# Kernel tuning notes

Hardware: AMD Instinct MI355X
Metric: run time of the kernel (lower is better)

## Reference

```python
import jax, jax.numpy as jnp
import numpy as np

EPSILON = 1e-6
MINMAX_RATIO = 20 ** 0.5
N_NODES, N_EDGES = 60000, 240000
WIDTH, NUM_HEAD, DIM_HEAD = 256, 8, 32
WIDTH_NORM = NUM_HEAD * DIM_HEAD          # 256
WIDTH_ACT = NUM_HEAD * DIM_HEAD * 4       # 1024
EDGE_VOCAB, EDGE_FEATS = 16, 3


def _inv_softplus(y):
    return np.log(np.expm1(y))


def setup_inputs() -> dict:
    key = jax.random.key(0)
    ks = jax.random.split(key, 16)
    inp = {
        'x': jax.random.normal(ks[0], (N_NODES, WIDTH), jnp.float32),
        'deg': jax.random.randint(ks[1], (N_NODES,), 0, 6, jnp.int32),
        'edge_idx': jax.random.randint(ks[2], (2, N_EDGES), 0, N_NODES, jnp.int32),
        'edge_attr': jax.random.randint(ks[3], (N_EDGES, EDGE_FEATS), 0, EDGE_VOCAB, jnp.int32),
        'node_elec': jax.random.normal(ks[4], (N_NODES, 2), jnp.float32),
        # parameters (init scales per module code)
        'lora_down': jax.random.normal(ks[5], (WIDTH, DIM_HEAD)) / np.sqrt(WIDTH),
        # original init is zeros; small random values used so this path is exercised
        'lora_up': jax.random.normal(ks[6], (DIM_HEAD, WIDTH_NORM)) * 0.01,
        'emb_edge': jax.random.normal(ks[7], (EDGE_VOCAB, DIM_HEAD)) * (0.01 / np.sqrt(EDGE_FEATS)),
        'moa_w': jnp.zeros((2, DIM_HEAD), jnp.float32),
        'moa_s': jnp.tile(jnp.linspace(float(_inv_softplus(0.1)), float(_inv_softplus(10.0)), DIM_HEAD), (2, 1)),
        'elec_lin': jax.random.normal(ks[8], (2, DIM_HEAD)) * (0.01 / np.sqrt(2)),
        'emb_deg': jax.random.normal(ks[9], (6, WIDTH_NORM)) * 0.1,
        'lin_pre': jax.random.normal(ks[10], (WIDTH, WIDTH_NORM)) / np.sqrt(WIDTH),
        'gate_lin': jax.random.normal(ks[11], (WIDTH_NORM, WIDTH_NORM)) / np.sqrt(WIDTH_NORM),
        'gate_kernel': jax.random.normal(ks[12], (NUM_HEAD, DIM_HEAD, DIM_HEAD * 4)) / np.sqrt(DIM_HEAD),
        'value_lin': jax.random.normal(ks[13], (WIDTH_NORM, WIDTH_NORM)) / np.sqrt(WIDTH_NORM),
        'value_kernel': jax.random.normal(ks[14], (NUM_HEAD, DIM_HEAD, DIM_HEAD * 4)) / np.sqrt(DIM_HEAD),
        'act_bias': jnp.full((WIDTH_ACT,), float(_inv_softplus(0.5)), jnp.float32),
        'post_kernel': jax.random.normal(ks[15], (NUM_HEAD, DIM_HEAD * 4, DIM_HEAD)) / np.sqrt(DIM_HEAD * 4),
    }
    return inp


def _clip_with_grad(x, lo, hi):
    return jax.lax.stop_gradient(jnp.clip(x, lo, hi) - x) + x


def _group_linear(x, lin_kernel, head_kernel, norm_bias=None):
    H, D, F = head_kernel.shape
    xx = (x @ lin_kernel).reshape(*x.shape[:-1], H, D)
    xx = xx / jnp.sqrt(jnp.mean(jnp.square(xx), axis=-1, keepdims=True) + EPSILON)
    if norm_bias is not None:
        xx = (xx + norm_bias.reshape(xx.shape)) / 2 ** 0.5
    xx = jnp.einsum('nhd,hdf->nhf', xx, head_kernel)
    return xx.reshape(*x.shape[:-1], H * F)


def reference(x, deg, edge_idx, edge_attr, node_elec, lora_down, lora_up, emb_edge,
              moa_w, moa_s, elec_lin, emb_deg, lin_pre, gate_lin, gate_kernel,
              value_lin, value_kernel, act_bias, post_kernel):
    ei0, ei1 = edge_idx[0], edge_idx[1]
    # edge embedding: bond features + electronegativity difference (MoAct tanh mixture)
    diff = node_elec[ei0] - node_elec[ei1]                      # [E,2]
    w = jax.nn.softplus(moa_w)
    w = w / w.sum(axis=-1, keepdims=True)
    s = jax.nn.softplus(moa_s)
    moa_out = (jnp.tanh(diff[..., None] * s) * w).sum(-1)       # [E,2]
    emb = jnp.sum(emb_edge[edge_attr], axis=-2) + moa_out @ elec_lin  # [E,dim_head]
    # per-edge message with LoRA modulation, scatter-add to destination nodes
    msg = x[ei0] + x[ei1]                                       # [E,width]
    msg = msg @ lin_pre + ((msg @ lora_down) * emb) @ lora_up   # [E,width_norm]
    agg = jax.ops.segment_sum(msg, ei1, num_segments=x.shape[0])
    # gated post-block with degree-embedding gate bias
    gate_bias = emb_deg[deg]                                    # [N,width_norm]
    gg = _group_linear(agg, gate_lin, gate_kernel, gate_bias)   # [N,width_act]
    vv = _group_linear(agg, value_lin, value_kernel)
    a = jax.nn.softplus(gg + act_bias)
    a = _clip_with_grad(a, 1.0 / MINMAX_RATIO, MINMAX_RATIO)
    xx = (a * vv).reshape(agg.shape[0], NUM_HEAD, -1)           # [N,H,4*dim_head]
    xx = jnp.einsum('nhd,hdf->nhf', xx, post_kernel)
    return xx.reshape(agg.shape[0], -1)                         # [N,width_norm]
```

## Files before the change

### kernel.cpp

```cpp
#include <hip/hip_runtime.h>
#include <hip/hip_bf16.h>

typedef unsigned short u16;

#define NN 60000
#define NE 240000

typedef __attribute__((ext_vector_type(8))) short bfrag;
typedef __attribute__((ext_vector_type(4))) float ffrag;

__device__ __forceinline__ float bf2f(u16 u) {
    union { unsigned int i; float f; } v; v.i = ((unsigned int)u) << 16; return v.f;
}
__device__ __forceinline__ u16 f2bf(float f) {
    __hip_bfloat16 h = __float2bfloat16(f);
    return *reinterpret_cast<u16*>(&h);
}
__device__ __forceinline__ float softplusf(float x) {
    return fmaxf(x, 0.f) + log1pf(expf(-fabsf(x)));
}
__device__ __forceinline__ float fast_softplus(float x) {
    return __logf(1.f + __expf(x));
}
__device__ __forceinline__ float fast_sp_clip(float x) {
    float a = __logf(1.f + __expf(x));
    return fminf(fmaxf(a, 0.22360679774997896f), 4.47213595499957939f);
}
__device__ __forceinline__ float fast_tanh(float x) {
    float t = __expf(fminf(fmaxf(2.f * x, -30.f), 30.f));
    return (t - 1.f) * __builtin_amdgcn_rcpf(t + 1.f);
}
template<bool B>
__device__ __forceinline__ float LD(const void* p, int i) {
    if constexpr (B) return bf2f(((const u16*)p)[i]);
    else             return ((const float*)p)[i];
}
__device__ __forceinline__ bfrag ldfrag(const u16* p) {
    return *reinterpret_cast<const bfrag*>(p);
}
__device__ __forceinline__ ffrag MFMA(bfrag a, bfrag b, ffrag c) {
    return __builtin_amdgcn_mfma_f32_16x16x32_bf16(a, b, c, 0, 0, 0);
}

__global__ void detect_kernel(const u16* __restrict__ x, int* __restrict__ flag) {
    __shared__ int cnt;
    if (threadIdx.x == 0) cnt = 0;
    __syncthreads();
    int c = 0;
    for (int i = threadIdx.x; i < 2048; i += 256) {
        u16 w = x[2 * i];
        int e = (w >> 7) & 0xFF;
        if (e >= 112 && e <= 143) c++;
    }
    atomicAdd(&cnt, c);
    __syncthreads();
    if (threadIdx.x == 0) *flag = (cnt > 1024) ? 1 : 0;
}

template<bool B>
__device__ void prep_body(const void* gate_lin, const void* value_lin,
    const void* lin_pre, const void* lora_down, const void* lora_up,
    const void* gate_kernel, const void* value_kernel, const void* post_kernel,
    u16* gT, u16* vT, u16* lpT, u16* ldT, u16* luT, u16* gkT, u16* vkT, u16* pkT,
    int tid, int stride)
{
    for (int i = tid; i < 65536; i += stride) {
        int n = i >> 8, k = i & 255;
        gT[i]  = f2bf(LD<B>(gate_lin,  k * 256 + n));
        vT[i]  = f2bf(LD<B>(value_lin, k * 256 + n));
        lpT[i] = f2bf(LD<B>(lin_pre,   k * 256 + n));
    }
    for (int i = tid; i < 8192; i += stride) {
        { int n = i >> 8, k = i & 255; ldT[i] = f2bf(LD<B>(lora_down, k * 32 + n)); }
        { int n = i >> 5, k = i & 31;  luT[i] = f2bf(LD<B>(lora_up,   k * 256 + n)); }
    }
    for (int i = tid; i < 32768; i += stride) {
        { int hf = i >> 5, d = i & 31, h = hf >> 7, f = hf & 127;
          gkT[i] = f2bf(LD<B>(gate_kernel,  h * 4096 + d * 128 + f));
          vkT[i] = f2bf(LD<B>(value_kernel, h * 4096 + d * 128 + f)); }
        { int hd = i >> 7, f = i & 127, h = hd >> 5, d2 = hd & 31;
          pkT[i] = f2bf(LD<B>(post_kernel, h * 4096 + f * 32 + d2)); }
    }
}
__global__ void prep_kernel(const void* gate_lin, const void* value_lin,
    const void* lin_pre, const void* lora_down, const void* lora_up,
    const void* gate_kernel, const void* value_kernel, const void* post_kernel,
    u16* gT, u16* vT, u16* lpT, u16* ldT, u16* luT, u16* gkT, u16* vkT, u16* pkT,
    const int* flag)
{
    int tid = blockIdx.x * blockDim.x + threadIdx.x;
    int stride = gridDim.x * blockDim.x;
    if (*flag) prep_body<true >(gate_lin, value_lin, lin_pre, lora_down, lora_up,
        gate_kernel, value_kernel, post_kernel, gT, vT, lpT, ldT, luT, gkT, vkT, pkT, tid, stride);
    else       prep_body<false>(gate_lin, value_lin, lin_pre, lora_down, lora_up,
        gate_kernel, value_kernel, post_kernel, gT, vT, lpT, ldT, luT, gkT, vkT, pkT, tid, stride);
}


struct PreSmem { __align__(16) u16 xB[64][264]; };

template<bool B>
__device__ void pre_body(PreSmem& sm, const void* x, const u16* ldT,
                         u16* xb, u16* xd, int blk, int j)
{
    const int w = j >> 6, quad = (j >> 4) & 3, l15 = j & 15;
    {
        int row = j >> 2, seg = j & 3, c0 = seg * 64;
        int gr = blk * 64 + row;
        if (gr < NN) {
            if constexpr (B) {
                const u16* xp = (const u16*)x + (size_t)gr * 256 + c0;
                for (int cc = 0; cc < 64; cc += 8)
                    *reinterpret_cast<bfrag*>(&sm.xB[row][c0 + cc]) = ldfrag(xp + cc);
            } else {
                const float* xp = (const float*)x + (size_t)gr * 256 + c0;
                u16* xbp = xb + (size_t)gr * 256 + c0;
                for (int cc = 0; cc < 64; cc += 8) {
                    float4 v0 = *(const float4*)(xp + cc);
                    float4 v1 = *(const float4*)(xp + cc + 4);
                    bfrag o;
                    o[0] = (short)f2bf(v0.x); o[1] = (short)f2bf(v0.y);
                    o[2] = (short)f2bf(v0.z); o[3] = (short)f2bf(v0.w);
                    o[4] = (short)f2bf(v1.x); o[5] = (short)f2bf(v1.y);
                    o[6] = (short)f2bf(v1.z); o[7] = (short)f2bf(v1.w);
                    *reinterpret_cast<bfrag*>(&sm.xB[row][c0 + cc]) = o;
                    *reinterpret_cast<bfrag*>(xbp + cc) = o;
                }
            }
        } else {
            bfrag z = {0,0,0,0,0,0,0,0};
            for (int cc = 0; cc < 64; cc += 8)
                *reinterpret_cast<bfrag*>(&sm.xB[row][c0 + cc]) = z;
        }
    }
    __syncthreads();
    const int r0 = w * 16;
    bfrag A[8];
    #pragma unroll
    for (int kt = 0; kt < 8; kt++)
        A[kt] = ldfrag(&sm.xB[r0 + l15][kt * 32 + quad * 8]);

    #pragma unroll
    for (int t = 0; t < 2; t++) {
        int n0 = t * 16;
        ffrag acc = {0.f, 0.f, 0.f, 0.f};
        #pragma unroll
        for (int kt = 0; kt < 8; kt++)
            acc = MFMA(A[kt], ldfrag(ldT + (n0 + l15) * 256 + kt * 32 + quad * 8), acc);
        #pragma unroll
        for (int r = 0; r < 4; r++) {
            int gr = blk * 64 + r0 + quad * 4 + r;
            if (gr < NN) xd[(size_t)gr * 32 + n0 + l15] = f2bf(acc[r]);
        }
    }
}
__global__ __launch_bounds__(256) void pre_kernel(const void* x, const u16* ldT,
    u16* xb, u16* xd, const int* flag)
{
    __shared__ PreSmem sm;
    const int j = threadIdx.x, blk = blockIdx.x;
    if (*flag) pre_body<true >(sm, x, ldT, xb, xd, blk, j);
    else       pre_body<false>(sm, x, ldT, xb, xd, blk, j);
}

__global__ __launch_bounds__(256) void hist_kernel(const int* __restrict__ edge_idx,
                                                   int* __restrict__ cnt)
{
    int e = blockIdx.x * blockDim.x + threadIdx.x;
    int stride = gridDim.x * blockDim.x;
    for (; e < NE; e += stride) atomicAdd(&cnt[edge_idx[NE + e]], 1);
}

__global__ __launch_bounds__(256) void scanA_kernel(const int* __restrict__ cnt,
                                                    int* __restrict__ bsum)
{
    __shared__ int sd[256];
    int b = blockIdx.x, j = threadIdx.x;
    int base = b * 1024 + j * 4;
    int s = 0;
    #pragma unroll
    for (int k = 0; k < 4; k++) { int i = base + k; if (i < NN) s += cnt[i]; }
    sd[j] = s; __syncthreads();
    for (int st = 128; st > 0; st >>= 1) {
        if (j < st) sd[j] += sd[j + st];
        __syncthreads();
    }
    if (j == 0) bsum[b] = sd[0];
}

__global__ __launch_bounds__(256) void scanB_kernel(const int* __restrict__ cnt,
    const int* __restrict__ bsum, int* __restrict__ off, int* __restrict__ cur)
{
    __shared__ int sd[256];
    int b = blockIdx.x, j = threadIdx.x;
    int pre = 0;
    for (int k = 0; k < b; k++) pre += bsum[k];
    int base = b * 1024 + j * 4;
    int c[4]; int tsum = 0;
    #pragma unroll
    for (int k = 0; k < 4; k++) { int i = base + k; c[k] = (i < NN) ? cnt[i] : 0; tsum += c[k]; }
    sd[j] = tsum; __syncthreads();
    for (int st = 1; st < 256; st <<= 1) {
        int v = (j >= st) ? sd[j - st] : 0;
        __syncthreads();
        sd[j] += v;
        __syncthreads();
    }
    int excl = sd[j] - tsum;
    int run = pre + excl;
    #pragma unroll
    for (int k = 0; k < 4; k++) {
        int i = base + k;
        if (i < NN) { off[i] = run; cur[i] = run; }
        run += c[k];
    }
}

struct EdgeWSmem {
    float wL[64], sL[64];
    float embT[512];
    float elT[64];
};

template<bool B>
__device__ void edgew_body(EdgeWSmem& sm, const int* edge_idx, const int* edge_attr,
    const void* node_elec, const void* emb_edge, const void* moa_w, const void* moa_s,
    const void* elec_lin, const u16* xd, u16* W, int* srcL, int* cur, int g, int j)
{
    if (j < 64) {
        int c = j >> 5;
        float sw = fast_softplus(LD<B>(moa_w, j));
        float tot = 0.f;
        #pragma unroll
        for (int d = 0; d < 32; d++) tot += fast_softplus(LD<B>(moa_w, c * 32 + d));
        sm.wL[j] = sw / tot;
        sm.sL[j] = fast_softplus(LD<B>(moa_s, j));
        sm.elT[j] = LD<B>(elec_lin, j);
    }
    for (int i = j; i < 512; i += 256) sm.embT[i] = LD<B>(emb_edge, i);
    __syncthreads();

    const int t = j & 3, s = j >> 2, e = g * 64 + s;
    const int a = edge_idx[e], b = edge_idx[NE + e];
    const int ch = t >> 1, dr = (t & 1) * 16;
    float df = LD<B>(node_elec, a * 2 + ch) - LD<B>(node_elec, b * 2 + ch);
    float part = 0.f;
    #pragma unroll
    for (int d = 0; d < 16; d++) {
        int dd = ch * 32 + dr + d;
        part += fast_tanh(df * sm.sL[dd]) * sm.wL[dd];
    }
    part += __shfl_xor(part, 1);
    int base = (j & 63) & ~3;
    float moa0 = __shfl(part, base + 0);
    float moa1 = __shfl(part, base + 2);

    int a0 = edge_attr[e * 3 + 0], a1 = edge_attr[e * 3 + 1], a2 = edge_attr[e * 3 + 2];
    int d0 = t * 8;
    bfrag va = ldfrag(xd + (size_t)a * 32 + d0);
    bfrag vb = ldfrag(xd + (size_t)b * 32 + d0);
    bfrag o;
    #pragma unroll
    for (int q = 0; q < 8; q++) {
        int d = d0 + q;
        float emb = sm.embT[a0 * 32 + d] + sm.embT[a1 * 32 + d] + sm.embT[a2 * 32 + d]
                  + moa0 * sm.elT[d] + moa1 * sm.elT[32 + d];
        o[q] = (short)f2bf((bf2f((u16)va[q]) + bf2f((u16)vb[q])) * emb);
    }
    int slot = 0;
    if (t == 0) slot = atomicAdd(&cur[b], 1);
    slot = __shfl(slot, base);
    if (t == 0) srcL[slot] = a;
    *reinterpret_cast<bfrag*>(W + (size_t)slot * 32 + d0) = o;
}

__global__ __launch_bounds__(256) void edgew_kernel(const int* edge_idx,
    const int* edge_attr, const void* node_elec, const void* emb_edge,
    const void* moa_w, const void* moa_s, const void* elec_lin,
    const u16* xd, u16* W, int* srcL, int* cur, const int* flag)
{
    __shared__ EdgeWSmem sm;
    const int j = threadIdx.x, g = blockIdx.x;
    if (*flag) edgew_body<true >(sm, edge_idx, edge_attr, node_elec, emb_edge,
                                 moa_w, moa_s, elec_lin, xd, W, srcL, cur, g, j);
    else       edgew_body<false>(sm, edge_idx, edge_attr, node_elec, emb_edge,
                                 moa_w, moa_s, elec_lin, xd, W, srcL, cur, g, j);
}

struct NodeSmemF {
    __align__(16) union U1 {
        u16 aggB[16][264];
        u16 ghatB[16][264];
    } u1;
    __align__(16) u16 sB[16][264];
    __align__(16) u16 xxW[4][16][136];
    __align__(16) u16 uB[16][40];
    int srcC[192];
    int degL[16], offL[16], idgL[16];
};

template<bool B>
__device__ void node_body_f(NodeSmemF& sm, const void* x, const u16* xb,
    const u16* Wb, const int* srcL, const int* off, const int* cnt, const int* deg,
    const void* emb_deg, const void* act_bias, const u16* gT, const u16* vT,
    const u16* gkT, const u16* vkT, const u16* pkT, const u16* lpT, const u16* luT,
    void* out, int blk, int j)
{
    const int w = j >> 6, quad = (j >> 4) & 3, l15 = j & 15;
    const int n0g = blk * 16;
    const u16* xbp = B ? (const u16*)x : xb;

    int o0 = off[n0g];
    int eb = off[n0g + 15] + cnt[n0g + 15] - o0;
    if (j < 192 && j < eb) sm.srcC[j] = srcL[o0 + j];
    if (j < 16) {
        sm.degL[j] = deg[n0g + j];
        sm.offL[j] = off[n0g + j];
        sm.idgL[j] = cnt[n0g + j];
    }
    __syncthreads();

    {
        int s = j >> 4, dp = j & 15, c0 = dp * 16;
        int o = sm.offL[s], dg = sm.idgL[s], base = o - o0;
        float acc[16];
        #pragma unroll
        for (int k = 0; k < 16; k++) acc[k] = 0.f;
        float u0 = 0.f, u1 = 0.f;
        bfrag pv0 = {0,0,0,0,0,0,0,0}, pv1 = {0,0,0,0,0,0,0,0};
        float pw0 = 0.f, pw1 = 0.f;
        if (dg > 0) {
            int src = (base < 192) ? sm.srcC[base] : srcL[o];
            const u16* xr = xbp + (size_t)src * 256 + c0;
            pv0 = ldfrag(xr); pv1 = ldfrag(xr + 8);
            const u16* wr = Wb + (size_t)o * 32 + dp;
            pw0 = bf2f(wr[0]); pw1 = bf2f(wr[16]);
        }
        for (int i = 0; i < dg; i++) {
            bfrag v0 = pv0, v1 = pv1;
            float w0 = pw0, w1 = pw1;
            if (i + 1 < dg) {
                int idx = base + i + 1;
                int src = (idx < 192) ? sm.srcC[idx] : srcL[o + i + 1];
                const u16* xr = xbp + (size_t)src * 256 + c0;
                pv0 = ldfrag(xr); pv1 = ldfrag(xr + 8);
                const u16* wr = Wb + (size_t)(o + i + 1) * 32 + dp;
                pw0 = bf2f(wr[0]); pw1 = bf2f(wr[16]);
            }
            u0 += w0; u1 += w1;
            #pragma unroll
            for (int q = 0; q < 8; q++) {
                acc[q]     += bf2f((u16)v0[q]);
                acc[q + 8] += bf2f((u16)v1[q]);
            }
        }
        {
            const u16* xr = xbp + (size_t)(n0g + s) * 256 + c0;
            bfrag v0 = ldfrag(xr), v1 = ldfrag(xr + 8);
            float fd = (float)dg;
            #pragma unroll
            for (int q = 0; q < 8; q++) {
                acc[q]     = fmaf(fd, bf2f((u16)v0[q]), acc[q]);
                acc[q + 8] = fmaf(fd, bf2f((u16)v1[q]), acc[q + 8]);
            }
        }
        sm.uB[s][dp] = f2bf(u0); sm.uB[s][dp + 16] = f2bf(u1);
        #pragma unroll
        for (int cq = 0; cq < 16; cq += 2) {
            unsigned int pv = (unsigned int)f2bf(acc[cq]) | ((unsigned int)f2bf(acc[cq + 1]) << 16);
            *reinterpret_cast<unsigned int*>(&sm.sB[s][c0 + cq]) = pv;
        }
    }
    __syncthreads();

    {
        bfrag S[8];
        #pragma unroll
        for (int kt = 0; kt < 8; kt++)
            S[kt] = ldfrag(&sm.sB[l15][kt * 32 + quad * 8]);
        bfrag uA = ldfrag(&sm.uB[l15][quad * 8]);
        #pragma unroll
        for (int tt = 0; tt < 4; tt++) {
            int n0 = (w * 4 + tt) * 16;
            const u16* bp = lpT + (n0 + l15) * 256 + quad * 8;
            bfrag b0 = ldfrag(bp +   0), b1 = ldfrag(bp +  32),
                  b2 = ldfrag(bp +  64), b3 = ldfrag(bp +  96),
                  b4 = ldfrag(bp + 128), b5 = ldfrag(bp + 160),
                  b6 = ldfrag(bp + 192), b7 = ldfrag(bp + 224);
            bfrag lu = ldfrag(luT + (n0 + l15) * 32 + quad * 8);
            ffrag acc = {0.f, 0.f, 0.f, 0.f};
            acc = MFMA(S[0], b0, acc); acc = MFMA(S[1], b1, acc);
            acc = MFMA(S[2], b2, acc); acc = MFMA(S[3], b3, acc);
            acc = MFMA(S[4], b4, acc); acc = MFMA(S[5], b5, acc);
            acc = MFMA(S[6], b6, acc); acc = MFMA(S[7], b7, acc);
            acc = MFMA(uA, lu, acc);
            #pragma unroll
            for (int r = 0; r < 4; r++)
                sm.u1.aggB[quad * 4 + r][n0 + l15] = f2bf(acc[r]);
        }
    }
    __syncthreads();

    {
        bfrag A[8];
        #pragma unroll
        for (int kt = 0; kt < 8; kt++)
            A[kt] = ldfrag(&sm.u1.aggB[l15][kt * 32 + quad * 8]);
        __syncthreads();

        const bool isG = (w >> 1) == 0;
        const u16* WT = isG ? gT : vT;
        const int half = (w & 1) * 128;
        #pragma unroll
        for (int hd = 0; hd < 4; hd++) {
            int n0 = half + hd * 32;
            ffrag a0 = {0.f, 0.f, 0.f, 0.f}, a1 = {0.f, 0.f, 0.f, 0.f};
            {
                const u16* bp = WT + (n0 + l15) * 256 + quad * 8;
                bfrag b0 = ldfrag(bp +   0), b1 = ldfrag(bp +  32),
                      b2 = ldfrag(bp +  64), b3 = ldfrag(bp +  96),
                      b4 = ldfrag(bp + 128), b5 = ldfrag(bp + 160),
                      b6 = ldfrag(bp + 192), b7 = ldfrag(bp + 224);
                a0 = MFMA(A[0], b0, a0); a0 = MFMA(A[1], b1, a0);
                a0 = MFMA(A[2], b2, a0); a0 = MFMA(A[3], b3, a0);
                a0 = MFMA(A[4], b4, a0); a0 = MFMA(A[5], b5, a0);
                a0 = MFMA(A[6], b6, a0); a0 = MFMA(A[7], b7, a0);
            }
            {
                const u16* bp = WT + (n0 + 16 + l15) * 256 + quad * 8;
                bfrag b0 = ldfrag(bp +   0), b1 = ldfrag(bp +  32),
                      b2 = ldfrag(bp +  64), b3 = ldfrag(bp +  96),
                      b4 = ldfrag(bp + 128), b5 = ldfrag(bp + 160),
                      b6 = ldfrag(bp + 192), b7 = ldfrag(bp + 224);
                a1 = MFMA(A[0], b0, a1); a1 = MFMA(A[1], b1, a1);
                a1 = MFMA(A[2], b2, a1); a1 = MFMA(A[3], b3, a1);
                a1 = MFMA(A[4], b4, a1); a1 = MFMA(A[5], b5, a1);
                a1 = MFMA(A[6], b6, a1); a1 = MFMA(A[7], b7, a1);
            }
            float inv[4];
            #pragma unroll
            for (int r = 0; r < 4; r++) {
                float sq = a0[r] * a0[r] + a1[r] * a1[r];
                sq += __shfl_xor(sq, 1);
                sq += __shfl_xor(sq, 2);
                sq += __shfl_xor(sq, 4);
                sq += __shfl_xor(sq, 8);
                inv[r] = 1.f / sqrtf(sq * (1.f / 32.f) + 1e-6f);
            }
            if (isG) {
                #pragma unroll
                for (int r = 0; r < 4; r++) {
                    int row = quad * 4 + r;
                    int dgr = sm.degL[row];
                    float b0 = LD<B>(emb_deg, dgr * 256 + n0 + l15);
                    float b1 = LD<B>(emb_deg, dgr * 256 + n0 + 16 + l15);
                    sm.u1.ghatB[row][n0 + l15] =
                        f2bf((a0[r] * inv[r] + b0) * 0.70710678118654752f);
                    sm.u1.ghatB[row][n0 + 16 + l15] =
                        f2bf((a1[r] * inv[r] + b1) * 0.70710678118654752f);
                }
            } else {
                #pragma unroll
                for (int r = 0; r < 4; r++) {
                    int row = quad * 4 + r;
                    sm.sB[row][n0 + l15]      = f2bf(a0[r] * inv[r]);
                    sm.sB[row][n0 + 16 + l15] = f2bf(a1[r] * inv[r]);
                }
            }
        }
    }
    __syncthreads();

    u16 (*xxW)[136] = sm.xxW[w];
    #pragma unroll
    for (int hh = 0; hh < 2; hh++) {
        int h = w * 2 + hh;
        bfrag aG = ldfrag(&sm.u1.ghatB[l15][h * 32 + quad * 8]);
        bfrag aV = ldfrag(&sm.sB[l15][h * 32 + quad * 8]);
        #pragma unroll
        for (int t = 0; t < 8; t++) {
            int n0 = t * 16;
            bfrag bg = ldfrag(gkT + (h * 128 + n0 + l15) * 32 + quad * 8);
            bfrag bv = ldfrag(vkT + (h * 128 + n0 + l15) * 32 + quad * 8);
            ffrag zero = {0.f, 0.f, 0.f, 0.f};
            ffrag ag = MFMA(aG, bg, zero);
            ffrag av = MFMA(aV, bv, zero);
            float bias = LD<B>(act_bias, h * 128 + n0 + l15);
            #pragma unroll
            for (int r = 0; r < 4; r++) {
                float a = fast_sp_clip(ag[r] + bias);
                xxW[quad * 4 + r][n0 + l15] = f2bf(a * av[r]);
            }
        }
        bfrag A4[4];
        #pragma unroll
        for (int kt = 0; kt < 4; kt++)
            A4[kt] = ldfrag(&xxW[l15][kt * 32 + quad * 8]);
        #pragma unroll
        for (int t = 0; t < 2; t++) {
            int n0 = t * 16;
            const u16* pp = pkT + (h * 32 + n0 + l15) * 128 + quad * 8;
            bfrag c0 = ldfrag(pp), c1 = ldfrag(pp + 32),
                  c2 = ldfrag(pp + 64), c3 = ldfrag(pp + 96);
            ffrag acc = {0.f, 0.f, 0.f, 0.f};
            acc = MFMA(A4[0], c0, acc); acc = MFMA(A4[1], c1, acc);
            acc = MFMA(A4[2], c2, acc); acc = MFMA(A4[3], c3, acc);
            #pragma unroll
            for (int r = 0; r < 4; r++) {
                size_t idx = (size_t)(n0g + quad * 4 + r) * 256 + h * 32 + n0 + l15;
                if constexpr (B) ((u16*)out)[idx] = f2bf(acc[r]);
                else             ((float*)out)[idx] = acc[r];
            }
        }
    }
}

__global__ __launch_bounds__(256, 4) void node_kernel_f(
    const void* x, const u16* xb, const u16* Wb, const int* srcL, const int* off,
    const int* cnt, const int* deg, const void* emb_deg, const void* act_bias,
    const u16* gT, const u16* vT, const u16* gkT, const u16* vkT, const u16* pkT,
    const u16* lpT, const u16* luT, void* out, const int* flag)
{
    __shared__ NodeSmemF sm;
    const int j = threadIdx.x, blk = blockIdx.x;
    if (*flag) node_body_f<true >(sm, x, xb, Wb, srcL, off, cnt, deg, emb_deg, act_bias,
                                  gT, vT, gkT, vkT, pkT, lpT, luT, out, blk, j);
    else       node_body_f<false>(sm, x, xb, Wb, srcL, off, cnt, deg, emb_deg, act_bias,
                                  gT, vT, gkT, vkT, pkT, lpT, luT, out, blk, j);
}

struct EdgeSmemM {
    __align__(16) u16 msgB[64][264];
    __align__(16) u16 uB[64][40];
    __align__(16) float embL[64][32];
    float wL[64], sL[64];
    float moaL[64][2];
    int ei0s[64], ei1s[64];
};

template<bool B>
__device__ void edge_body_m(EdgeSmemM& sm, const void* x, const int* edge_idx,
    const int* edge_attr, const void* node_elec, const void* emb_edge,
    const void* moa_w, const void* moa_s, const void* elec_lin,
    const u16* ldT, const u16* luT, const u16* lpT, float* agg, int g, int j)
{
    const int w = j >> 6, quad = (j >> 4) & 3, l15 = j & 15;
    const int lane = j & 63;

    if (w == 0) {
        int c = lane >> 5;
        float sw = softplusf(LD<B>(moa_w, lane));
        float tot = 0.f;
        #pragma unroll
        for (int d = 0; d < 32; d++) tot += softplusf(LD<B>(moa_w, c * 32 + d));
        sm.wL[lane] = sw / tot;
        sm.sL[lane] = softplusf(LD<B>(moa_s, lane));
        int e = g * 64 + lane;
        int a = edge_idx[e], b = edge_idx[NE + e];
        sm.ei0s[lane] = a; sm.ei1s[lane] = b;
        #pragma unroll
        for (int c2 = 0; c2 < 2; c2++) {
            float df = LD<B>(node_elec, a * 2 + c2) - LD<B>(node_elec, b * 2 + c2);
            float acc = 0.f;
            for (int d = 0; d < 32; d++)
                acc += tanhf(df * sm.sL[c2 * 32 + d]) * sm.wL[c2 * 32 + d];
            sm.moaL[lane][c2] = acc;
        }
    }
    __syncthreads();

    {
        int row = j >> 2, seg = j & 3, c0 = seg * 64;
        int e0 = sm.ei0s[row], e1 = sm.ei1s[row];
        if constexpr (B) {
            const u16* xp = (const u16*)x;
            for (int cc = 0; cc < 64; cc += 8) {
                bfrag v0 = ldfrag(xp + (size_t)e0 * 256 + c0 + cc);
                bfrag v1 = ldfrag(xp + (size_t)e1 * 256 + c0 + cc);
                bfrag o;
                #pragma unroll
                for (int q = 0; q < 8; q++)
                    o[q] = (short)f2bf(bf2f((u16)v0[q]) + bf2f((u16)v1[q]));
                *reinterpret_cast<bfrag*>(&sm.msgB[row][c0 + cc]) = o;
            }
        } else {
            const float* xp = (const float*)x;
            for (int cc = 0; cc < 64; cc += 4) {
                float4 v0 = *(const float4*)(xp + (size_t)e0 * 256 + c0 + cc);
                float4 v1 = *(const float4*)(xp + (size_t)e1 * 256 + c0 + cc);
                ushort4 o = { f2bf(v0.x + v1.x), f2bf(v0.y + v1.y),
                              f2bf(v0.z + v1.z), f2bf(v0.w + v1.w) };
                *reinterpret_cast<ushort4*>(&sm.msgB[row][c0 + cc]) = o;
            }
        }
        int e = row, d0 = seg * 8, ea = g * 64 + e;
        int a0 = edge_attr[ea * 3 + 0], a1 = edge_attr[ea * 3 + 1], a2 = edge_attr[ea * 3 + 2];
        float m0 = sm.moaL[e][0], m1 = sm.moaL[e][1];
        #pragma unroll
        for (int d = d0; d < d0 + 8; d++) {
            sm.embL[e][d] = LD<B>(emb_edge, a0 * 32 + d) + LD<B>(emb_edge, a1 * 32 + d)
                          + LD<B>(emb_edge, a2 * 32 + d)
                          + m0 * LD<B>(elec_lin, d) + m1 * LD<B>(elec_lin, 32 + d);
        }
    }
    __syncthreads();

    const int r0 = w * 16;
    bfrag A[8];
    #pragma unroll
    for (int kt = 0; kt < 8; kt++)
        A[kt] = ldfrag(&sm.msgB[r0 + l15][kt * 32 + quad * 8]);

    #pragma unroll
    for (int t = 0; t < 2; t++) {
        int n0 = t * 16;
        ffrag acc = {0.f, 0.f, 0.f, 0.f};
        #pragma unroll
        for (int kt = 0; kt < 8; kt++)
            acc = MFMA(A[kt], ldfrag(ldT + (n0 + l15) * 256 + kt * 32 + quad * 8), acc);
        #pragma unroll
        for (int r = 0; r < 4; r++) {
            int row = r0 + quad * 4 + r;
            sm.uB[row][n0 + l15] = f2bf(acc[r] * sm.embL[row][n0 + l15]);
        }
    }
    bfrag uA = ldfrag(&sm.uB[r0 + l15][quad * 8]);

    int er[4];
    #pragma unroll
    for (int r = 0; r < 4; r++) er[r] = sm.ei1s[r0 + quad * 4 + r];

    for (int t = 0; t < 16; t++) {
        int n0 = t * 16;
        ffrag acc = {0.f, 0.f, 0.f, 0.f};
        #pragma unroll
        for (int kt = 0; kt < 8; kt++)
            acc = MFMA(A[kt], ldfrag(lpT + (n0 + l15) * 256 + kt * 32 + quad * 8), acc);
        acc = MFMA(uA, ldfrag(luT + (n0 + l15) * 32 + quad * 8), acc);
        #pragma unroll
        for (int r = 0; r < 4; r++)
            unsafeAtomicAdd(&agg[(size_t)er[r] * 256 + n0 + l15], acc[r]);
    }
}

__global__ __launch_bounds__(256) void edge_kernel_m(
    const void* x, const int* edge_idx, const int* edge_attr,
    const void* node_elec, const void* emb_edge, const void* moa_w,
    const void* moa_s, const void* elec_lin,
    const u16* ldT, const u16* luT, const u16* lpT, float* agg, const int* flag)
{
    __shared__ EdgeSmemM sm;
    const int j = threadIdx.x, g = blockIdx.x;
    if (*flag) edge_body_m<true >(sm, x, edge_idx, edge_attr, node_elec, emb_edge,
                                  moa_w, moa_s, elec_lin, ldT, luT, lpT, agg, g, j);
    else       edge_body_m<false>(sm, x, edge_idx, edge_attr, node_elec, emb_edge,
                                  moa_w, moa_s, elec_lin, ldT, luT, lpT, agg, g, j);
}

struct NodeSmemM {
    union U1 {
        u16 aggB[16][264];
        u16 ghatB[16][264];
    } u1;
    union U2 {
        struct P { float gF[16][260]; float vF[16][260]; } p;
        u16 xxB[16][1032];
    } u2;
    __align__(16) u16 vhatB[16][264];
    float grmsL[16][8], vrmsL[16][8];
    int degL[16];
};

template<bool B>
__device__ void node_body_m(NodeSmemM& sm, const float* agg, const int* deg,
    const void* emb_deg, const void* act_bias, const u16* gT, const u16* vT,
    const u16* gkT, const u16* vkT, const u16* pkT, void* out, int blk, int j)
{
    const int w = j >> 6, quad = (j >> 4) & 3, l15 = j & 15;
    const int n0g = blk * 16;

// ... 206 lines not shown
    for (int s = 0; s < 8; s++)
        unsafeAtomicAdd(&agg[(size_t)sm.ei1s[s] * 256 + j], acc[s]);
}

__global__ __launch_bounds__(256) void edge_kernel_fb(
    const void* x, const int* edge_idx, const int* edge_attr,
    const void* node_elec, const void* lora_down, const void* lora_up,
    const void* emb_edge, const void* moa_w, const void* moa_s,
    const void* elec_lin, const void* lin_pre, float* agg, const int* flag)
{
    __shared__ EdgeSmemFB sm;
    const int j = threadIdx.x, g = blockIdx.x;
    if (*flag) edge_body_fb<true >(sm, x, edge_idx, edge_attr, node_elec, lora_down,
                                   lora_up, emb_edge, moa_w, moa_s, elec_lin, lin_pre, agg, g, j);
    else       edge_body_fb<false>(sm, x, edge_idx, edge_attr, node_elec, lora_down,
                                   lora_up, emb_edge, moa_w, moa_s, elec_lin, lin_pre, agg, g, j);
}

struct NodeSmemFB {
    __align__(16) float aggT[256][8];
    float gL[8][256];
    float vL[8][256];
    float ghat[256], vhat[256];
    float xxL[1024];
};

template<bool B>
__device__ void node_body_fb(NodeSmemFB& sm,
    const float* agg, const int* deg, const void* emb_deg,
    const void* gate_lin, const void* value_lin, const void* gate_kernel,
    const void* value_kernel, const void* act_bias, const void* post_kernel,
    void* out, int n0, int j)
{
    #pragma unroll
    for (int s = 0; s < 8; s++) sm.aggT[j][s] = agg[(size_t)(n0 + s) * 256 + j];
    __syncthreads();

    float ga[8], va[8];
    #pragma unroll
    for (int s = 0; s < 8; s++) { ga[s] = 0.f; va[s] = 0.f; }
    #pragma unroll 4
    for (int k = 0; k < 256; k++) {
        float wg = LD<B>(gate_lin,  k * 256 + j);
        float wv = LD<B>(value_lin, k * 256 + j);
        const float4 a0 = *reinterpret_cast<const float4*>(&sm.aggT[k][0]);
        const float4 a1 = *reinterpret_cast<const float4*>(&sm.aggT[k][4]);
        ga[0] = fmaf(a0.x, wg, ga[0]); va[0] = fmaf(a0.x, wv, va[0]);
        ga[1] = fmaf(a0.y, wg, ga[1]); va[1] = fmaf(a0.y, wv, va[1]);
        ga[2] = fmaf(a0.z, wg, ga[2]); va[2] = fmaf(a0.z, wv, va[2]);
        ga[3] = fmaf(a0.w, wg, ga[3]); va[3] = fmaf(a0.w, wv, va[3]);
        ga[4] = fmaf(a1.x, wg, ga[4]); va[4] = fmaf(a1.x, wv, va[4]);
        ga[5] = fmaf(a1.y, wg, ga[5]); va[5] = fmaf(a1.y, wv, va[5]);
        ga[6] = fmaf(a1.z, wg, ga[6]); va[6] = fmaf(a1.z, wv, va[6]);
        ga[7] = fmaf(a1.w, wg, ga[7]); va[7] = fmaf(a1.w, wv, va[7]);
    }
    __syncthreads();
    #pragma unroll
    for (int s = 0; s < 8; s++) { sm.gL[s][j] = ga[s]; sm.vL[s][j] = va[s]; }

    const int h = j >> 5, dd = j & 31, f0 = dd << 2;
    const float lo = 0.22360679774997896f, hi = 4.47213595499957939f;

    for (int s = 0; s < 8; s++) {
        __syncthreads();
        float gs = 0.f, vs = 0.f;
        #pragma unroll
        for (int d = 0; d < 32; d++) {
            float g = sm.gL[s][h * 32 + d];
            float v = sm.vL[s][h * 32 + d];
            gs = fmaf(g, g, gs); vs = fmaf(v, v, vs);
        }
        float grms = sqrtf(gs * (1.f / 32.f) + 1e-6f);
        float vrms = sqrtf(vs * (1.f / 32.f) + 1e-6f);
        float gv = sm.gL[s][j], vv = sm.vL[s][j];
        float bias = LD<B>(emb_deg, deg[n0 + s] * 256 + j);
        sm.ghat[j] = (gv / grms + bias) * 0.70710678118654752f;
        sm.vhat[j] = vv / vrms;
        __syncthreads();

        float a0 = 0.f, a1 = 0.f, a2 = 0.f, a3 = 0.f;
        float b0 = 0.f, b1 = 0.f, b2 = 0.f, b3 = 0.f;
        #pragma unroll 4
        for (int d = 0; d < 32; d++) {
            float gh = sm.ghat[h * 32 + d];
            float vh = sm.vhat[h * 32 + d];
            int base = h * 4096 + d * 128 + f0;
            a0 = fmaf(gh, LD<B>(gate_kernel,  base + 0), a0);
            a1 = fmaf(gh, LD<B>(gate_kernel,  base + 1), a1);
            a2 = fmaf(gh, LD<B>(gate_kernel,  base + 2), a2);
            a3 = fmaf(gh, LD<B>(gate_kernel,  base + 3), a3);
            b0 = fmaf(vh, LD<B>(value_kernel, base + 0), b0);
            b1 = fmaf(vh, LD<B>(value_kernel, base + 1), b1);
            b2 = fmaf(vh, LD<B>(value_kernel, base + 2), b2);
            b3 = fmaf(vh, LD<B>(value_kernel, base + 3), b3);
        }
        int fb = h * 128 + f0;
        a0 = fminf(fmaxf(softplusf(a0 + LD<B>(act_bias, fb + 0)), lo), hi);
        a1 = fminf(fmaxf(softplusf(a1 + LD<B>(act_bias, fb + 1)), lo), hi);
        a2 = fminf(fmaxf(softplusf(a2 + LD<B>(act_bias, fb + 2)), lo), hi);
        a3 = fminf(fmaxf(softplusf(a3 + LD<B>(act_bias, fb + 3)), lo), hi);
        sm.xxL[fb + 0] = a0 * b0; sm.xxL[fb + 1] = a1 * b1;
        sm.xxL[fb + 2] = a2 * b2; sm.xxL[fb + 3] = a3 * b3;
        __syncthreads();

        float o = 0.f;
        #pragma unroll 4
        for (int f = 0; f < 128; f++)
            o = fmaf(sm.xxL[h * 128 + f], LD<B>(post_kernel, h * 4096 + f * 32 + dd), o);
        if constexpr (B) ((u16*)out)[(size_t)(n0 + s) * 256 + j] = f2bf(o);
        else             ((float*)out)[(size_t)(n0 + s) * 256 + j] = o;
    }
}

__global__ __launch_bounds__(256) void node_kernel_fb(
    const float* agg, const int* deg, const void* emb_deg,
    const void* gate_lin, const void* value_lin, const void* gate_kernel,
    const void* value_kernel, const void* act_bias, const void* post_kernel,
    void* out, const int* flag)
{
    __shared__ NodeSmemFB sm;
    const int j = threadIdx.x, n0 = blockIdx.x * 8;
    if (*flag) node_body_fb<true >(sm, agg, deg, emb_deg, gate_lin, value_lin,
                                   gate_kernel, value_kernel, act_bias, post_kernel, out, n0, j);
    else       node_body_fb<false>(sm, agg, deg, emb_deg, gate_lin, value_lin,
                                   gate_kernel, value_kernel, act_bias, post_kernel, out, n0, j);
}

extern "C" void kernel_launch(void* const* d_in, const int* in_sizes, int n_in,
                              void* d_out, int out_size, void* d_ws, size_t ws_size,
                              hipStream_t stream) {
    const void* x           = d_in[0];
    const int*  deg         = (const int*)d_in[1];
    const int*  edge_idx    = (const int*)d_in[2];
    const int*  edge_attr   = (const int*)d_in[3];
    const void* node_elec   = d_in[4];
    const void* lora_down   = d_in[5];
    const void* lora_up     = d_in[6];
    const void* emb_edge    = d_in[7];
    const void* moa_w       = d_in[8];
    const void* moa_s       = d_in[9];
    const void* elec_lin    = d_in[10];
    const void* emb_deg     = d_in[11];
    const void* lin_pre     = d_in[12];
    const void* gate_lin    = d_in[13];
    const void* gate_kernel = d_in[14];
    const void* value_lin   = d_in[15];
    const void* value_kernel= d_in[16];
    const void* act_bias    = d_in[17];
    const void* post_kernel = d_in[18];

    const size_t AGG_BYTES = (size_t)NN * 256 * 4;
    const size_t T_BYTES   = (size_t)(3 * 65536 + 2 * 8192 + 3 * 32768) * 2;

    const size_t XB_OFF  = 16 + T_BYTES;
    const size_t W_OFF   = XB_OFF  + (size_t)NN * 256 * 2;
    const size_t XD_OFF  = W_OFF   + (size_t)NE * 32 * 2;
    const size_t SRC_OFF = XD_OFF  + (size_t)NN * 32 * 2;
    const size_t CNT_OFF = SRC_OFF + (size_t)NE * 4;
    const size_t OFF_OFF = CNT_OFF + (size_t)NN * 4;
    const size_t CUR_OFF = OFF_OFF + (size_t)NN * 4;
    const size_t BS_OFF  = CUR_OFF + (size_t)NN * 4;
    const size_t NEW_NEEDED = BS_OFF + 256;

    const size_t T_OFF_OLD  = AGG_BYTES + 16;
    const size_t OLD_NEEDED = T_OFF_OLD + T_BYTES;

    if (ws_size >= NEW_NEEDED) {
        int* flag = (int*)d_ws;
        u16* gT  = (u16*)((char*)d_ws + 16);
        u16* vT  = gT  + 65536;
        u16* lpT = vT  + 65536;
        u16* ldT = lpT + 65536;
        u16* luT = ldT + 8192;
        u16* gkT = luT + 8192;
        u16* vkT = gkT + 32768;
        u16* pkT = vkT + 32768;
        u16*  xb   = (u16*)((char*)d_ws + XB_OFF);
        u16*  Wb   = (u16*)((char*)d_ws + W_OFF);
        u16*  xd   = (u16*)((char*)d_ws + XD_OFF);
        int* srcL  = (int*)((char*)d_ws + SRC_OFF);
        int* cnt   = (int*)((char*)d_ws + CNT_OFF);
        int* offA  = (int*)((char*)d_ws + OFF_OFF);
        int* cur   = (int*)((char*)d_ws + CUR_OFF);
        int* bsum  = (int*)((char*)d_ws + BS_OFF);

        detect_kernel<<<1, 256, 0, stream>>>((const u16*)x, flag);
        prep_kernel<<<128, 256, 0, stream>>>(
            gate_lin, value_lin, lin_pre, lora_down, lora_up,
            gate_kernel, value_kernel, post_kernel,
            gT, vT, lpT, ldT, luT, gkT, vkT, pkT, flag);
        hipMemsetAsync(cnt, 0, (size_t)NN * 4, stream);
        pre_kernel<<<(NN + 63) / 64, 256, 0, stream>>>(x, ldT, xb, xd, flag);
        hist_kernel<<<256, 256, 0, stream>>>(edge_idx, cnt);
        scanA_kernel<<<59, 256, 0, stream>>>(cnt, bsum);
        scanB_kernel<<<59, 256, 0, stream>>>(cnt, bsum, offA, cur);
        edgew_kernel<<<NE / 64, 256, 0, stream>>>(
            edge_idx, edge_attr, node_elec, emb_edge, moa_w, moa_s, elec_lin,
            xd, Wb, srcL, cur, flag);
        node_kernel_f<<<NN / 16, 256, 0, stream>>>(
            x, xb, Wb, srcL, offA, cnt, deg, emb_deg, act_bias,
            gT, vT, gkT, vkT, pkT, lpT, luT, d_out, flag);
    } else if (ws_size >= OLD_NEEDED) {
        float* agg = (float*)d_ws;
        int* flag  = (int*)((char*)d_ws + AGG_BYTES);
        u16* gT  = (u16*)((char*)d_ws + T_OFF_OLD);
        u16* vT  = gT  + 65536;
        u16* lpT = vT  + 65536;
        u16* ldT = lpT + 65536;
        u16* luT = ldT + 8192;
        u16* gkT = luT + 8192;
        u16* vkT = gkT + 32768;
        u16* pkT = vkT + 32768;

        hipMemsetAsync(agg, 0, AGG_BYTES, stream);
        detect_kernel<<<1, 256, 0, stream>>>((const u16*)x, flag);
        prep_kernel<<<128, 256, 0, stream>>>(
            gate_lin, value_lin, lin_pre, lora_down, lora_up,
            gate_kernel, value_kernel, post_kernel,
            gT, vT, lpT, ldT, luT, gkT, vkT, pkT, flag);
        edge_kernel_m<<<NE / 64, 256, 0, stream>>>(
            x, edge_idx, edge_attr, node_elec, emb_edge, moa_w, moa_s, elec_lin,
            ldT, luT, lpT, agg, flag);
        node_kernel_m<<<NN / 16, 256, 0, stream>>>(
            agg, deg, emb_deg, act_bias, gT, vT, gkT, vkT, pkT, d_out, flag);
    } else {
        float* agg = (float*)d_ws;
        int* flag  = (int*)((char*)d_ws + AGG_BYTES);
        hipMemsetAsync(agg, 0, AGG_BYTES, stream);
        detect_kernel<<<1, 256, 0, stream>>>((const u16*)x, flag);
        edge_kernel_fb<<<NE / 8, 256, 0, stream>>>(
            x, edge_idx, edge_attr, node_elec, lora_down, lora_up, emb_edge,
            moa_w, moa_s, elec_lin, lin_pre, agg, flag);
        node_kernel_fb<<<NN / 8, 256, 0, stream>>>(
            agg, deg, emb_deg, gate_lin, value_lin, gate_kernel, value_kernel,
            act_bias, post_kernel, d_out, flag);
    }
}
```

Baseline: 484.5 us.

## Split neighbor gather into separate kernel and drop bf16 copy of x

The edge gather/aggregation moves out of the heavy node kernel into its own gather kernel. That kernel reads x directly (fp32 when the input is fp32), writes the bf16 aggregated sums S and LoRA sums U, and the node kernel then just loads them. This removes the xb bf16 conversion write in pre_kernel and decouples the latency-bound gather from the register-heavy MFMA node kernel, which runs at launch_bounds occupancy 4. In exchange it adds an extra kernel launch and a round trip of S and U through global memory. The fp32 gather also reads twice the bytes per neighbor row.

```diff
diff --git a/kernel.cpp b/kernel.cpp
--- a/kernel.cpp
+++ b/kernel.cpp
@@ -101,7 +101,7 @@
 
 template<bool B>
 __device__ void pre_body(PreSmem& sm, const void* x, const u16* ldT,
-                         u16* xb, u16* xd, int blk, int j)
+                         u16* xd, int blk, int j)
 {
     const int w = j >> 6, quad = (j >> 4) & 3, l15 = j & 15;
     {
@@ -114,7 +114,6 @@
                     *reinterpret_cast<bfrag*>(&sm.xB[row][c0 + cc]) = ldfrag(xp + cc);
             } else {
                 const float* xp = (const float*)x + (size_t)gr * 256 + c0;
-                u16* xbp = xb + (size_t)gr * 256 + c0;
                 for (int cc = 0; cc < 64; cc += 8) {
                     float4 v0 = *(const float4*)(xp + cc);
                     float4 v1 = *(const float4*)(xp + cc + 4);
@@ -124,7 +123,6 @@
                     o[4] = (short)f2bf(v1.x); o[5] = (short)f2bf(v1.y);
                     o[6] = (short)f2bf(v1.z); o[7] = (short)f2bf(v1.w);
                     *reinterpret_cast<bfrag*>(&sm.xB[row][c0 + cc]) = o;
-                    *reinterpret_cast<bfrag*>(xbp + cc) = o;
                 }
             }
         } else {
@@ -155,12 +153,12 @@
     }
 }
 __global__ __launch_bounds__(256) void pre_kernel(const void* x, const u16* ldT,
-    u16* xb, u16* xd, const int* flag)
+    u16* xd, const int* flag)
 {
     __shared__ PreSmem sm;
     const int j = threadIdx.x, blk = blockIdx.x;
-    if (*flag) pre_body<true >(sm, x, ldT, xb, xd, blk, j);
-    else       pre_body<false>(sm, x, ldT, xb, xd, blk, j);
+    if (*flag) pre_body<true >(sm, x, ldT, xd, blk, j);
+    else       pre_body<false>(sm, x, ldT, xd, blk, j);
 }
 
 __global__ __launch_bounds__(256) void hist_kernel(const int* __restrict__ edge_idx,
@@ -285,6 +283,134 @@
                                  moa_w, moa_s, elec_lin, xd, W, srcL, cur, g, j);
     else       edgew_body<false>(sm, edge_idx, edge_attr, node_elec, emb_edge,
                                  moa_w, moa_s, elec_lin, xd, W, srcL, cur, g, j);
+}
+
+struct GatherSmem {
+    int srcC[192];
+    int offL[16], idgL[16];
+};
+
+template<bool B>
+__device__ void gather_body(GatherSmem& sm, const void* x, const u16* Wb,
+    const int* srcL, const int* off, const int* cnt,
+    u16* S, u16* U, int blk, int j)
+{
+    const int n0g = blk * 16;
+    int o0 = off[n0g];
+    int eb = off[n0g + 15] + cnt[n0g + 15] - o0;
+    if (j < 192 && j < eb) sm.srcC[j] = srcL[o0 + j];
+    if (j < 16) { sm.offL[j] = off[n0g + j]; sm.idgL[j] = cnt[n0g + j]; }
+    __syncthreads();
+
+    const int s = j >> 4, dp = j & 15, c0 = dp * 16;
+    const int o = sm.offL[s], dg = sm.idgL[s], base = o - o0;
+    float acc[16];
+    #pragma unroll
+    for (int k = 0; k < 16; k++) acc[k] = 0.f;
+    float u0 = 0.f, u1 = 0.f;
+
+    if constexpr (B) {
+        const u16* xp = (const u16*)x;
+        bfrag pv0 = {0,0,0,0,0,0,0,0}, pv1 = {0,0,0,0,0,0,0,0};
+        float pw0 = 0.f, pw1 = 0.f;
+        if (dg > 0) {
+            int src = (base < 192) ? sm.srcC[base] : srcL[o];
+            const u16* xr = xp + (size_t)src * 256 + c0;
+            pv0 = ldfrag(xr); pv1 = ldfrag(xr + 8);
+            const u16* wr = Wb + (size_t)o * 32 + dp;
+            pw0 = bf2f(wr[0]); pw1 = bf2f(wr[16]);
+        }
+        for (int i = 0; i < dg; i++) {
+            bfrag v0 = pv0, v1 = pv1;
+            float w0 = pw0, w1 = pw1;
+            if (i + 1 < dg) {
+                int idx = base + i + 1;
+                int src = (idx < 192) ? sm.srcC[idx] : srcL[o + i + 1];
+                const u16* xr = xp + (size_t)src * 256 + c0;
+                pv0 = ldfrag(xr); pv1 = ldfrag(xr + 8);
+                const u16* wr = Wb + (size_t)(o + i + 1) * 32 + dp;
+                pw0 = bf2f(wr[0]); pw1 = bf2f(wr[16]);
+            }
+            u0 += w0; u1 += w1;
+            #pragma unroll
+            for (int q = 0; q < 8; q++) {
+                acc[q]     += bf2f((u16)v0[q]);
+                acc[q + 8] += bf2f((u16)v1[q]);
+            }
+        }
+        {
+            const u16* xr = xp + (size_t)(n0g + s) * 256 + c0;
+            bfrag v0 = ldfrag(xr), v1 = ldfrag(xr + 8);
+            float fd = (float)dg;
+            #pragma unroll
+            for (int q = 0; q < 8; q++) {
+                acc[q]     = fmaf(fd, bf2f((u16)v0[q]), acc[q]);
+                acc[q + 8] = fmaf(fd, bf2f((u16)v1[q]), acc[q + 8]);
+            }
+        }
+    } else {
+        const float* xp = (const float*)x;
+        float4 p0 = {0,0,0,0}, p1 = {0,0,0,0}, p2 = {0,0,0,0}, p3 = {0,0,0,0};
+        float pw0 = 0.f, pw1 = 0.f;
+        if (dg > 0) {
+            int src = (base < 192) ? sm.srcC[base] : srcL[o];
+            const float* r = xp + (size_t)src * 256 + c0;
+            p0 = *(const float4*)r;       p1 = *(const float4*)(r + 4);
+            p2 = *(const float4*)(r + 8); p3 = *(const float4*)(r + 12);
+            const u16* wr = Wb + (size_t)o * 32 + dp;
+            pw0 = bf2f(wr[0]); pw1 = bf2f(wr[16]);
+        }
+        for (int i = 0; i < dg; i++) {
+            float4 a0 = p0, a1 = p1, a2 = p2, a3 = p3;
+            float w0 = pw0, w1 = pw1;
+            if (i + 1 < dg) {
+                int idx = base + i + 1;
+                int src = (idx < 192) ? sm.srcC[idx] : srcL[o + i + 1];
+                const float* r = xp + (size_t)src * 256 + c0;
+                p0 = *(const float4*)r;       p1 = *(const float4*)(r + 4);
+                p2 = *(const float4*)(r + 8); p3 = *(const float4*)(r + 12);
+                const u16* wr = Wb + (size_t)(o + i + 1) * 32 + dp;
+                pw0 = bf2f(wr[0]); pw1 = bf2f(wr[16]);
+            }
+            u0 += w0; u1 += w1;
+            acc[0]  += a0.x; acc[1]  += a0.y; acc[2]  += a0.z; acc[3]  += a0.w;
+            acc[4]  += a1.x; acc[5]  += a1.y; acc[6]  += a1.z; acc[7]  += a1.w;
+            acc[8]  += a2.x; acc[9]  += a2.y; acc[10] += a2.z; acc[11] += a2.w;
+            acc[12] += a3.x; acc[13] += a3.y; acc[14] += a3.z; acc[15] += a3.w;
+        }
+        {
+            const float* r = xp + (size_t)(n0g + s) * 256 + c0;
+            float4 a0 = *(const float4*)r,       a1 = *(const float4*)(r + 4);
+            float4 a2 = *(const float4*)(r + 8), a3 = *(const float4*)(r + 12);
+            float fd = (float)dg;
+            acc[0]  = fmaf(fd, a0.x, acc[0]);  acc[1]  = fmaf(fd, a0.y, acc[1]);
+            acc[2]  = fmaf(fd, a0.z, acc[2]);  acc[3]  = fmaf(fd, a0.w, acc[3]);
+            acc[4]  = fmaf(fd, a1.x, acc[4]);  acc[5]  = fmaf(fd, a1.y, acc[5]);
+            acc[6]  = fmaf(fd, a1.z, acc[6]);  acc[7]  = fmaf(fd, a1.w, acc[7]);
+            acc[8]  = fmaf(fd, a2.x, acc[8]);  acc[9]  = fmaf(fd, a2.y, acc[9]);
+            acc[10] = fmaf(fd, a2.z, acc[10]); acc[11] = fmaf(fd, a2.w, acc[11]);
+            acc[12] = fmaf(fd, a3.x, acc[12]); acc[13] = fmaf(fd, a3.y, acc[13]);
+            acc[14] = fmaf(fd, a3.z, acc[14]); acc[15] = fmaf(fd, a3.w, acc[15]);
+        }
+    }
+
+    u16* Sp = S + (size_t)(n0g + s) * 256 + c0;
+    #pragma unroll
+    for (int cq = 0; cq < 16; cq += 2) {
+        unsigned int pv = (unsigned int)f2bf(acc[cq]) | ((unsigned int)f2bf(acc[cq + 1]) << 16);
+        *reinterpret_cast<unsigned int*>(Sp + cq) = pv;
+    }
+    U[(size_t)(n0g + s) * 32 + dp]      = f2bf(u0);
+    U[(size_t)(n0g + s) * 32 + dp + 16] = f2bf(u1);
+}
+
+__global__ __launch_bounds__(256) void gather_kernel(const void* x, const u16* Wb,
+    const int* srcL, const int* off, const int* cnt, u16* S, u16* U, const int* flag)
+{
+    __shared__ GatherSmem sm;
+    const int j = threadIdx.x, blk = blockIdx.x;
+    if (*flag) gather_body<true >(sm, x, Wb, srcL, off, cnt, S, U, blk, j);
+    else       gather_body<false>(sm, x, Wb, srcL, off, cnt, S, U, blk, j);
 }
 
 struct NodeSmemF {
@@ -295,89 +421,35 @@
     __align__(16) u16 sB[16][264];
     __align__(16) u16 xxW[4][16][136];
     __align__(16) u16 uB[16][40];
-    int srcC[192];
-    int degL[16], offL[16], idgL[16];
+    int degL[16];
 };
 
 template<bool B>
-__device__ void node_body_f(NodeSmemF& sm, const void* x, const u16* xb,
-    const u16* Wb, const int* srcL, const int* off, const int* cnt, const int* deg,
-    const void* emb_deg, const void* act_bias, const u16* gT, const u16* vT,
-    const u16* gkT, const u16* vkT, const u16* pkT, const u16* lpT, const u16* luT,
-    void* out, int blk, int j)
+__device__ void node_body_f(NodeSmemF& sm, const u16* S, const u16* U,
+    const int* deg, const void* emb_deg, const void* act_bias,
+    const u16* gT, const u16* vT, const u16* gkT, const u16* vkT, const u16* pkT,
+    const u16* lpT, const u16* luT, void* out, int blk, int j)
 {
     const int w = j >> 6, quad = (j >> 4) & 3, l15 = j & 15;
     const int n0g = blk * 16;
-    const u16* xbp = B ? (const u16*)x : xb;
-
-    int o0 = off[n0g];
-    int eb = off[n0g + 15] + cnt[n0g + 15] - o0;
-    if (j < 192 && j < eb) sm.srcC[j] = srcL[o0 + j];
-    if (j < 16) {
-        sm.degL[j] = deg[n0g + j];
-        sm.offL[j] = off[n0g + j];
-        sm.idgL[j] = cnt[n0g + j];
-    }
-    __syncthreads();
 
     {
-        int s = j >> 4, dp = j & 15, c0 = dp * 16;
-        int o = sm.offL[s], dg = sm.idgL[s], base = o - o0;
-        float acc[16];
-        #pragma unroll
-        for (int k = 0; k < 16; k++) acc[k] = 0.f;
-        float u0 = 0.f, u1 = 0.f;
-        bfrag pv0 = {0,0,0,0,0,0,0,0}, pv1 = {0,0,0,0,0,0,0,0};
-        float pw0 = 0.f, pw1 = 0.f;
-        if (dg > 0) {
-            int src = (base < 192) ? sm.srcC[base] : srcL[o];
-            const u16* xr = xbp + (size_t)src * 256 + c0;
-            pv0 = ldfrag(xr); pv1 = ldfrag(xr + 8);
-            const u16* wr = Wb + (size_t)o * 32 + dp;
-            pw0 = bf2f(wr[0]); pw1 = bf2f(wr[16]);
-        }
-        for (int i = 0; i < dg; i++) {
-            bfrag v0 = pv0, v1 = pv1;
-            float w0 = pw0, w1 = pw1;
-            if (i + 1 < dg) {
-                int idx = base + i + 1;
-                int src = (idx < 192) ? sm.srcC[idx] : srcL[o + i + 1];
-                const u16* xr = xbp + (size_t)src * 256 + c0;
-                pv0 = ldfrag(xr); pv1 = ldfrag(xr + 8);
-                const u16* wr = Wb + (size_t)(o + i + 1) * 32 + dp;
-                pw0 = bf2f(wr[0]); pw1 = bf2f(wr[16]);
-            }
-            u0 += w0; u1 += w1;
-            #pragma unroll
-            for (int q = 0; q < 8; q++) {
-                acc[q]     += bf2f((u16)v0[q]);
-                acc[q + 8] += bf2f((u16)v1[q]);
-            }
-        }
-        {
-            const u16* xr = xbp + (size_t)(n0g + s) * 256 + c0;
-            bfrag v0 = ldfrag(xr), v1 = ldfrag(xr + 8);
-            float fd = (float)dg;
-            #pragma unroll
-            for (int q = 0; q < 8; q++) {
-                acc[q]     = fmaf(fd, bf2f((u16)v0[q]), acc[q]);
-                acc[q + 8] = fmaf(fd, bf2f((u16)v1[q]), acc[q + 8]);
-            }
-        }
-        sm.uB[s][dp] = f2bf(u0); sm.uB[s][dp + 16] = f2bf(u1);
-        #pragma unroll
-        for (int cq = 0; cq < 16; cq += 2) {
-            unsigned int pv = (unsigned int)f2bf(acc[cq]) | ((unsigned int)f2bf(acc[cq + 1]) << 16);
-            *reinterpret_cast<unsigned int*>(&sm.sB[s][c0 + cq]) = pv;
-        }
+        int row = j >> 4, c0 = (j & 15) * 16;
+        const u16* Sp = S + (size_t)(n0g + row) * 256 + c0;
+        *reinterpret_cast<bfrag*>(&sm.sB[row][c0])     = ldfrag(Sp);
+        *reinterpret_cast<bfrag*>(&sm.sB[row][c0 + 8]) = ldfrag(Sp + 8);
+        int d = j & 15;
+        sm.uB[row][d]      = U[(size_t)(n0g + row) * 32 + d];
+        sm.uB[row][d + 16] = U[(size_t)(n0g + row) * 32 + d + 16];
+        if (j < 16) sm.degL[j] = deg[n0g + j];
     }
     __syncthreads();
 
     {
-        bfrag S[8];
+        bfrag Sf[8];
         #pragma unroll
         for (int kt = 0; kt < 8; kt++)
-            S[kt] = ldfrag(&sm.sB[l15][kt * 32 + quad * 8]);
+            Sf[kt] = ldfrag(&sm.sB[l15][kt * 32 + quad * 8]);
         bfrag uA = ldfrag(&sm.uB[l15][quad * 8]);
         #pragma unroll
         for (int tt = 0; tt < 4; tt++) {
@@ -389,10 +461,10 @@
                   b6 = ldfrag(bp + 192), b7 = ldfrag(bp + 224);
             bfrag lu = ldfrag(luT + (n0 + l15) * 32 + quad * 8);
             ffrag acc = {0.f, 0.f, 0.f, 0.f};
-            acc = MFMA(S[0], b0, acc); acc = MFMA(S[1], b1, acc);
-            acc = MFMA(S[2], b2, acc); acc = MFMA(S[3], b3, acc);
-            acc = MFMA(S[4], b4, acc); acc = MFMA(S[5], b5, acc);
-            acc = MFMA(S[6], b6, acc); acc = MFMA(S[7], b7, acc);
+            acc = MFMA(Sf[0], b0, acc); acc = MFMA(Sf[1], b1, acc);
+            acc = MFMA(Sf[2], b2, acc); acc = MFMA(Sf[3], b3, acc);
+            acc = MFMA(Sf[4], b4, acc); acc = MFMA(Sf[5], b5, acc);
+            acc = MFMA(Sf[6], b6, acc); acc = MFMA(Sf[7], b7, acc);
             acc = MFMA(uA, lu, acc);
             #pragma unroll
             for (int r = 0; r < 4; r++)
@@ -516,16 +588,16 @@
 }
 
 __global__ __launch_bounds__(256, 4) void node_kernel_f(
-    const void* x, const u16* xb, const u16* Wb, const int* srcL, const int* off,
-    const int* cnt, const int* deg, const void* emb_deg, const void* act_bias,
-    const u16* gT, const u16* vT, const u16* gkT, const u16* vkT, const u16* pkT,
-    const u16* lpT, const u16* luT, void* out, const int* flag)
+    const u16* S, const u16* U, const int* deg, const void* emb_deg,
+    const void* act_bias, const u16* gT, const u16* vT, const u16* gkT,
+    const u16* vkT, const u16* pkT, const u16* lpT, const u16* luT,
+    void* out, const int* flag)
 {
     __shared__ NodeSmemF sm;
     const int j = threadIdx.x, blk = blockIdx.x;
-    if (*flag) node_body_f<true >(sm, x, xb, Wb, srcL, off, cnt, deg, emb_deg, act_bias,
+    if (*flag) node_body_f<true >(sm, S, U, deg, emb_deg, act_bias,
                                   gT, vT, gkT, vkT, pkT, lpT, luT, out, blk, j);
-    else       node_body_f<false>(sm, x, xb, Wb, srcL, off, cnt, deg, emb_deg, act_bias,
+    else       node_body_f<false>(sm, S, U, deg, emb_deg, act_bias,
                                   gT, vT, gkT, vkT, pkT, lpT, luT, out, blk, j);
 }
 
@@ -1038,10 +1110,11 @@
     const size_t AGG_BYTES = (size_t)NN * 256 * 4;
     const size_t T_BYTES   = (size_t)(3 * 65536 + 2 * 8192 + 3 * 32768) * 2;
 
-    const size_t XB_OFF  = 16 + T_BYTES;
-    const size_t W_OFF   = XB_OFF  + (size_t)NN * 256 * 2;
+    const size_t S_OFF   = 16 + T_BYTES;
+    const size_t W_OFF   = S_OFF   + (size_t)NN * 256 * 2;
     const size_t XD_OFF  = W_OFF   + (size_t)NE * 32 * 2;
-    const size_t SRC_OFF = XD_OFF  + (size_t)NN * 32 * 2;
+    const size_t U_OFF   = XD_OFF  + (size_t)NN * 32 * 2;
+    const size_t SRC_OFF = U_OFF   + (size_t)NN * 32 * 2;
     const size_t CNT_OFF = SRC_OFF + (size_t)NE * 4;
     const size_t OFF_OFF = CNT_OFF + (size_t)NN * 4;
     const size_t CUR_OFF = OFF_OFF + (size_t)NN * 4;
@@ -1061,9 +1134,10 @@
         u16* gkT = luT + 8192;
         u16* vkT = gkT + 32768;
         u16* pkT = vkT + 32768;
-        u16*  xb   = (u16*)((char*)d_ws + XB_OFF);
+        u16*  S    = (u16*)((char*)d_ws + S_OFF);
         u16*  Wb   = (u16*)((char*)d_ws + W_OFF);
         u16*  xd   = (u16*)((char*)d_ws + XD_OFF);
+        u16*  U    = (u16*)((char*)d_ws + U_OFF);
         int* srcL  = (int*)((char*)d_ws + SRC_OFF);
         int* cnt   = (int*)((char*)d_ws + CNT_OFF);
         int* offA  = (int*)((char*)d_ws + OFF_OFF);
@@ -1076,15 +1150,17 @@
             gate_kernel, value_kernel, post_kernel,
             gT, vT, lpT, ldT, luT, gkT, vkT, pkT, flag);
         hipMemsetAsync(cnt, 0, (size_t)NN * 4, stream);
-        pre_kernel<<<(NN + 63) / 64, 256, 0, stream>>>(x, ldT, xb, xd, flag);
+        pre_kernel<<<(NN + 63) / 64, 256, 0, stream>>>(x, ldT, xd, flag);
         hist_kernel<<<256, 256, 0, stream>>>(edge_idx, cnt);
         scanA_kernel<<<59, 256, 0, stream>>>(cnt, bsum);
         scanB_kernel<<<59, 256, 0, stream>>>(cnt, bsum, offA, cur);
         edgew_kernel<<<NE / 64, 256, 0, stream>>>(
             edge_idx, edge_attr, node_elec, emb_edge, moa_w, moa_s, elec_lin,
             xd, Wb, srcL, cur, flag);
+        gather_kernel<<<NN / 16, 256, 0, stream>>>(
+            x, Wb, srcL, offA, cnt, S, U, flag);
         node_kernel_f<<<NN / 16, 256, 0, stream>>>(
-            x, xb, Wb, srcL, offA, cnt, deg, emb_deg, act_bias,
+            S, U, deg, emb_deg, act_bias,
             gT, vT, gkT, vkT, pkT, lpT, luT, d_out, flag);
     } else if (ws_size >= OLD_NEEDED) {
         float* agg = (float*)d_ws;
```

New measurement: 485.4 us. No clear change (+0.2%).
